# Kernel optimization log

Hardware: AMD Instinct MI355X
Metric: run time of the kernel (lower is better)

Reference implementation:

```python
import jax, jax.numpy as jnp
import numpy as np

N, D, E, TOP_K = 2048, 512, 16, 2
HID = 4 * D
EPS = 1e-10


def setup_inputs() -> dict:
    key = jax.random.key(0)
    ks = jax.random.split(key, 8)
    s = 0.02
    return {
        "x": jax.random.normal(ks[0], (N, D), dtype=jnp.float32),
        "w_norm": jnp.ones((D,), dtype=jnp.float32),
        "Wr": jax.random.normal(ks[1], (D, E), dtype=jnp.float32) * s,
        "br": jnp.zeros((E,), dtype=jnp.float32),
        "W1": jax.random.normal(ks[2], (E, D, HID), dtype=jnp.float32) * s,
        "b1": jnp.zeros((E, HID), dtype=jnp.float32),
        "W2": jax.random.normal(ks[3], (E, HID, D), dtype=jnp.float32) * s,
        "b2": jnp.zeros((E, D), dtype=jnp.float32),
    }


def reference(x, w_norm, Wr, br, W1, b1, W2, b2):
    res = x
    # RMSNorm over feature dim (dim=1 in the torch code for 2D input)
    rms = jnp.sqrt(jnp.mean(x * x, axis=1, keepdims=True) + EPS)
    xn = w_norm * (x / rms)
    # Router: top-k over expert logits, softmax over the k selected logits
    logits = xn @ Wr + br                      # [N, E]
    top_p, top_i = jax.lax.top_k(logits, TOP_K)  # [N, k]
    top_p = jax.nn.softmax(top_p, axis=-1)
    # Dense per-token expert weights [N, E] (top-k indices are distinct)
    weight = jnp.zeros((x.shape[0], E), dtype=x.dtype)
    weight = weight.at[jnp.arange(x.shape[0])[:, None], top_i].add(top_p)
    # All-expert FFN (dense reference for the routed dispatch)
    h = jnp.einsum("nd,edh->enh", xn, W1) + b1[:, None, :]   # [E, N, 4D]
    y = jnp.einsum("enh,ehd->end", jax.nn.silu(h), W2) + b2[:, None, :]  # [E, N, D]
    out = jnp.einsum("end,ne->nd", y, weight)
    return out + res
```

## Files before the change

kernel.cpp:

```cpp
#include <hip/hip_runtime.h>

#define N_TOK 2048
#define DIM   512
#define NEXP  16
#define HID   2048
#define NSLOT (N_TOK*2)

typedef __attribute__((ext_vector_type(8))) short short8;
typedef __attribute__((ext_vector_type(4))) float floatx4;

__device__ __forceinline__ ushort f2bf(float f) {
    union { float f; unsigned u; } c; c.f = f;
    unsigned u = c.u;
    unsigned r = (u + 0x7fffu + ((u >> 16) & 1u)) >> 16;
    return (ushort)r;
}
__device__ __forceinline__ float bf2f(ushort u) {
    union { unsigned u; float f; } c; c.u = ((unsigned)u) << 16;
    return c.f;
}

__device__ __forceinline__ void gl_lds16(const void* g, void* l) {
    __builtin_amdgcn_global_load_lds(
        (const __attribute__((address_space(1))) unsigned int*)g,
        (__attribute__((address_space(3))) unsigned int*)l, 16, 0, 0);
}

__device__ __forceinline__ void transpose_tile(const float* __restrict__ src,
                                               ushort* __restrict__ dst,
                                               int K, int Nn, int bx, void* smem)
{
    float* Ls = (float*)smem;
    const int NT = Nn >> 6;
    const int KT = K >> 6;
    const int nt = bx % NT; bx /= NT;
    const int kt = bx % KT; bx /= KT;
    const int e  = bx;
    const int t = threadIdx.x;

    const float* sp = src + ((size_t)e * K + kt * 64) * Nn + nt * 64;
#pragma unroll
    for (int i = 0; i < 4; i++) {
        const int k  = (t >> 4) + i * 16;
        const int c4 = (t & 15) * 4;
        const float4 v = *(const float4*)(sp + (size_t)k * Nn + c4);
        Ls[k * 65 + c4 + 0] = v.x;
        Ls[k * 65 + c4 + 1] = v.y;
        Ls[k * 65 + c4 + 2] = v.z;
        Ls[k * 65 + c4 + 3] = v.w;
    }
    __syncthreads();

    ushort* dp = dst + ((size_t)e * Nn + nt * 64) * K + kt * 64;
#pragma unroll
    for (int i = 0; i < 2; i++) {
        const int n = (t >> 3) + i * 32;
        const int c = t & 7;
        unsigned w[4];
#pragma unroll
        for (int q = 0; q < 4; q++) {
            const unsigned lo = f2bf(Ls[(c * 8 + q * 2 + 0) * 65 + n]);
            const unsigned hi = f2bf(Ls[(c * 8 + q * 2 + 1) * 65 + n]);
            w[q] = lo | (hi << 16);
        }
        uint4 o = make_uint4(w[0], w[1], w[2], w[3]);
        *(uint4*)(dp + (size_t)n * K + c * 8) = o;
    }
}

__global__ __launch_bounds__(256)
void router_fused(const float* __restrict__ x, const float* __restrict__ w_norm,
                  const float* __restrict__ Wr, const float* __restrict__ br,
                  ushort* __restrict__ xn, int2* __restrict__ rec_e,
                  float2* __restrict__ rec_w)
{
    __shared__ float xs[16][516];
    __shared__ float wrT[16][516];

    const int tid  = threadIdx.x;
    const int wave = tid >> 6, lane = tid & 63;
    const int tblk = blockIdx.x * 16;

#pragma unroll
    for (int k = 0; k < 32; k++) {
        const int idx = tid + k * 256;
        wrT[idx & 15][idx >> 4] = Wr[idx];
    }

    const float4* wnp = (const float4*)w_norm;
    const float4 wa = wnp[lane], wb = wnp[lane + 64];
#pragma unroll
    for (int i = 0; i < 4; i++) {
        const int tl = wave * 4 + i, t = tblk + tl;
        const float4* xp = (const float4*)(x + (size_t)t * DIM);
        const float4 a = xp[lane], b = xp[lane + 64];
        float ss = a.x*a.x + a.y*a.y + a.z*a.z + a.w*a.w
                 + b.x*b.x + b.y*b.y + b.z*b.z + b.w*b.w;
#pragma unroll
        for (int m = 32; m >= 1; m >>= 1) ss += __shfl_xor(ss, m, 64);
        const float rinv = 1.f / sqrtf(ss * (1.f / (float)DIM) + 1e-10f);
        float4 na, nb;
        na.x = a.x * wa.x * rinv; na.y = a.y * wa.y * rinv;
        na.z = a.z * wa.z * rinv; na.w = a.w * wa.w * rinv;
        nb.x = b.x * wb.x * rinv; nb.y = b.y * wb.y * rinv;
        nb.z = b.z * wb.z * rinv; nb.w = b.w * wb.w * rinv;
        *(float4*)&xs[tl][lane * 4]       = na;
        *(float4*)&xs[tl][256 + lane * 4] = nb;
        ushort4 ua, ub;
        ua.x = f2bf(na.x); ua.y = f2bf(na.y); ua.z = f2bf(na.z); ua.w = f2bf(na.w);
        ub.x = f2bf(nb.x); ub.y = f2bf(nb.y); ub.z = f2bf(nb.z); ub.w = f2bf(nb.w);
        ushort4* xo = (ushort4*)(xn + (size_t)t * DIM);
        xo[lane] = ua; xo[lane + 64] = ub;
    }
    __syncthreads();

    const int tl = tid >> 4, e = tid & 15;
    const int t = tblk + tl;
    float acc = 0.f;
#pragma unroll 4
    for (int d = 0; d < DIM; d += 4) {
        const float4 xv = *(const float4*)&xs[tl][d];
        const float4 wv = *(const float4*)&wrT[e][d];
        acc += xv.x * wv.x + xv.y * wv.y + xv.z * wv.z + xv.w * wv.w;
    }
    const float v = acc + br[e];

    float m0 = v; int i0 = e; float m1 = -1e30f; int i1 = 16;
#pragma unroll
    for (int msk = 1; msk < 16; msk <<= 1) {
        const float om0 = __shfl_xor(m0, msk, 64); const int oi0 = __shfl_xor(i0, msk, 64);
        const float om1 = __shfl_xor(m1, msk, 64); const int oi1 = __shfl_xor(i1, msk, 64);
        const bool bf_ = (om0 > m0) || (om0 == m0 && oi0 < i0);
        const float t0m = bf_ ? om0 : m0; const int t0i = bf_ ? oi0 : i0;
        const float l0m = bf_ ? m0 : om0; const int l0i = bf_ ? i0 : oi0;
        const bool b2_ = (om1 > m1) || (om1 == m1 && oi1 < i1);
        const float t2m = b2_ ? om1 : m1; const int t2i = b2_ ? oi1 : i1;
        const bool lw = (l0m > t2m) || (l0m == t2m && l0i < t2i);
        m0 = t0m; i0 = t0i;
        m1 = lw ? l0m : t2m; i1 = lw ? l0i : t2i;
    }
    if (e == 0) {
        const float ex = expf(m1 - m0);
        const float w0 = 1.f / (1.f + ex);
        rec_e[t] = make_int2(i0, i1);
        rec_w[t] = make_float2(w0, ex * w0);
    }
}

__global__ __launch_bounds__(1024)
void plan_kernel(const int2* __restrict__ rec_e, int* __restrict__ cnt,
                 int* __restrict__ off, int* __restrict__ tok_of_slot,
                 int* __restrict__ rec_slot)
{
    __shared__ int soff[17];
    const int e = threadIdx.x >> 6;
    const int lane = threadIdx.x & 63;

    int total = 0;
    for (int c = 0; c < N_TOK / 64; c++) {
        const int2 er = rec_e[c * 64 + lane];
        const bool hit = (er.x == e) || (er.y == e);
        total += __popcll(__ballot(hit));
    }
    if (lane == 0) soff[e + 1] = total;
    __syncthreads();
    if (threadIdx.x == 0) {
        soff[0] = 0;
        for (int q = 1; q <= 16; q++) soff[q] += soff[q - 1];
    }
    __syncthreads();
    int base = soff[e];
    if (lane == 0) { cnt[e] = soff[e + 1] - base; off[e] = base; }

    for (int c = 0; c < N_TOK / 64; c++) {
        const int t = c * 64 + lane;
        const int2 er = rec_e[t];
        const bool hit = (er.x == e) || (er.y == e);
        const unsigned long long b = __ballot(hit);
        if (hit) {
            const int slot = base + __popcll(b & ((1ull << lane) - 1ull));
            tok_of_slot[slot] = t;
            const int which = (er.y == e) ? 1 : 0;
            rec_slot[t * 2 + which] = slot;
        }
        base += __popcll(b);
    }
}

__global__ __launch_bounds__(256)
void gemm1_trw2(const ushort* __restrict__ A,
                const float* __restrict__ W1, const float* __restrict__ b1,
                const int* __restrict__ cnt, const int* __restrict__ off,
                const int* __restrict__ tok_of_slot,
                ushort* __restrict__ hout,
                const float* __restrict__ w2src, ushort* __restrict__ w2dst)
{
    __shared__ __align__(16) char smem[33280];

    if (blockIdx.y >= 64) {
        const int bx = (blockIdx.y - 64) * 32 + blockIdx.x;
        transpose_tile(w2src, w2dst, HID, DIM, bx, smem);
        return;
    }

    const int flat = blockIdx.x + (blockIdx.y << 5);
    const int x = flat & 7;
    const int g = flat >> 3;
    const int e  = x + ((g >> 7) << 3);
    const int r0_ = g & 127;
    const int nb = r0_ & 31, mt = r0_ >> 5;

    const int count = cnt[e];
    if (mt * 128 >= count) return;
    const int base = off[e];
    const int rows = min(128, count - mt * 128);
    const int n0   = nb * 64;

    ushort* As_ = (ushort*)smem;
    float*  Bf_ = (float*)(smem + 16384);
    int*    toks = (int*)(smem + 32768);

    const int tid = threadIdx.x;
    if (tid < 128) {
        const int r = tid < rows ? tid : rows - 1;
        toks[tid] = tok_of_slot[base + mt * 128 + r];
    }
    __syncthreads();

    const int lane = tid & 63;
    const int wid  = tid >> 6;
    const int wm = wid >> 1, wn = wid & 1;
    const int fr = lane & 15, fg = lane >> 4;

    const int rl  = lane >> 2;
    const int sko = ((lane & 3) ^ ((lane >> 4) & 3)) * 8;

    const ushort* aptr[2];
#pragma unroll
    for (int j = 0; j < 2; j++) {
        const int s = wid * 2 + j;
        aptr[j] = A + (size_t)toks[s * 16 + rl] * DIM + sko;
    }
    const float* bptr[2];
#pragma unroll
    for (int j = 0; j < 2; j++) {
        const int s = wid * 2 + j;
        const int cs = ((lane & 15) * 4) ^ (((s >> 1) & 1) << 4);
        bptr[j] = W1 + ((size_t)e * DIM + s * 4 + (lane >> 4)) * HID + n0 + cs;
    }

    floatx4 acc[4][2];
#pragma unroll
    for (int mi = 0; mi < 4; mi++)
#pragma unroll
        for (int ni = 0; ni < 2; ni++)
#pragma unroll
            for (int r = 0; r < 4; r++) acc[mi][ni][r] = 0.f;

#define STAGE1(pb, ktn)                                                            \
    do {                                                                           \
        const int ka = (ktn) * 32;                                                 \
        const size_t kb = (size_t)(ktn) * 32 * HID;                                \
        _Pragma("unroll")                                                          \
        for (int j = 0; j < 2; j++)                                                \
            gl_lds16(aptr[j] + ka, (void*)(&As_[(pb) * 4096 + (wid * 2 + j) * 512])); \
        _Pragma("unroll")                                                          \
        for (int j = 0; j < 2; j++)                                                \
            gl_lds16(bptr[j] + kb, (void*)(&Bf_[(pb) * 2048 + (wid * 2 + j) * 256])); \
    } while (0)

    int cur = 0;
    STAGE1(0, 0);

    const int cxor = (fr >> 2) & 3;
    const int bbase = wn * 32 + fr;
    const int fgx = fg & 1;
    for (int kt = 0; kt < 16; kt++) {
        if (kt < 15) {
            STAGE1(cur ^ 1, kt + 1);
            asm volatile("s_waitcnt vmcnt(4)" ::: "memory");
        } else {
            asm volatile("s_waitcnt vmcnt(0)" ::: "memory");
        }
        __builtin_amdgcn_s_barrier();
        __builtin_amdgcn_sched_barrier(0);

        __builtin_amdgcn_s_setprio(1);
        {
            const int co = (fg ^ cxor) * 8;
            short8 af[4], bfr[2];
#pragma unroll
            for (int mi = 0; mi < 4; mi++)
                af[mi] = *(const short8*)&As_[cur * 4096 + (wm * 64 + mi * 16 + fr) * 32 + co];
#pragma unroll
            for (int ni = 0; ni < 2; ni++) {
                const int pcol = bbase + ((ni ^ fgx) << 4);
#pragma unroll
                for (int j = 0; j < 8; j++) {
                    const float f = Bf_[cur * 2048 + (fg * 8 + j) * 64 + pcol];
                    bfr[ni][j] = (short)f2bf(f);
                }
            }
#pragma unroll
            for (int mi = 0; mi < 4; mi++)
#pragma unroll
                for (int ni = 0; ni < 2; ni++)
                    acc[mi][ni] = __builtin_amdgcn_mfma_f32_16x16x32_bf16(af[mi], bfr[ni], acc[mi][ni], 0, 0, 0);
        }
        __builtin_amdgcn_s_setprio(0);

        __builtin_amdgcn_sched_barrier(0);
        __builtin_amdgcn_s_barrier();
        cur ^= 1;
    }
#undef STAGE1

#pragma unroll
    for (int ni = 0; ni < 2; ni++) {
        const int gn = n0 + wn * 32 + ni * 16 + fr;
        const float bv = b1[e * HID + gn];
#pragma unroll
        for (int mi = 0; mi < 4; mi++) {
#pragma unroll
            for (int r = 0; r < 4; r++) {
                const int lm = wm * 64 + mi * 16 + fg * 4 + r;
                if (lm < rows) {
                    const int slot = base + mt * 128 + lm;
                    float v = acc[mi][ni][r] + bv;
                    v = v / (1.f + __expf(-v));
                    hout[(size_t)slot * HID + gn] = f2bf(v);
                }
            }
        }
    }
}

__global__ __launch_bounds__(256)
void gemm2_kernel(const ushort* __restrict__ A,
                  const ushort* __restrict__ WT,
                  const int* __restrict__ cnt, const int* __restrict__ off,
                  ushort* __restrict__ yout)
{
    const int flat = blockIdx.x + (blockIdx.y << 5);
    const int x = flat & 7;
    const int g = flat >> 3;
    const int G = ((g >> 5) << 3) + x;
    const int e = G >> 2, z = G & 3;
    const int idx = g & 31;
    const int mt = idx >> 3, nb = idx & 7;

    const int count = cnt[e];
    if (mt * 128 >= count) return;
    const int base = off[e];
    const int rows = min(128, count - mt * 128);
    const int n0   = nb * 64;
    const int kbeg = z * 512;
    ushort* yp = yout + (size_t)z * NSLOT * DIM;

    __shared__ __align__(16) ushort As[2][128 * 32];
    __shared__ __align__(16) ushort Bs[2][64 * 32];
    __shared__ int toks[128];

    const int tid = threadIdx.x;
    if (tid < 128) {
        const int r = tid < rows ? tid : rows - 1;
        toks[tid] = base + mt * 128 + r;
    }
    __syncthreads();

    const int lane = tid & 63;
    const int wid  = tid >> 6;
    const int wm = wid >> 1, wn = wid & 1;
    const int fr = lane & 15, fg = lane >> 4;

    const int rl  = lane >> 2;
    const int sko = ((lane & 3) ^ ((lane >> 4) & 3)) * 8;

    const ushort* aptr[2];
#pragma unroll
    for (int j = 0; j < 2; j++) {
        const int s = wid * 2 + j;
        aptr[j] = A + (size_t)toks[s * 16 + rl] * HID + kbeg + sko;
    }
    const ushort* bptr = WT + ((size_t)e * DIM + n0 + wid * 16 + rl) * HID + kbeg + sko;

    floatx4 acc[4][2];
#pragma unroll
    for (int mi = 0; mi < 4; mi++)
#pragma unroll
        for (int ni = 0; ni < 2; ni++)
#pragma unroll
            for (int r = 0; r < 4; r++) acc[mi][ni][r] = 0.f;

#define STAGE2(pb, k0)                                                       \
    do {                                                                     \
        _Pragma("unroll")                                                    \
        for (int j = 0; j < 2; j++)                                          \
            gl_lds16(aptr[j] + (k0), (void*)(&As[pb][(wid * 2 + j) * 512])); \
        gl_lds16(bptr + (k0), (void*)(&Bs[pb][wid * 512]));                  \
    } while (0)

    int cur = 0;
    STAGE2(0, 0);

    const int cxor = (fr >> 2) & 3;
    for (int kt = 0; kt < 16; kt++) {
        if (kt < 15) {
            STAGE2(cur ^ 1, (kt + 1) * 32);
            asm volatile("s_waitcnt vmcnt(3)" ::: "memory");
        } else {
            asm volatile("s_waitcnt vmcnt(0)" ::: "memory");
        }
        __builtin_amdgcn_s_barrier();
        __builtin_amdgcn_sched_barrier(0);

        __builtin_amdgcn_s_setprio(1);
        {
            const int co = (fg ^ cxor) * 8;
            short8 af[4], bfr[2];
#pragma unroll
            for (int mi = 0; mi < 4; mi++)
                af[mi] = *(const short8*)&As[cur][(wm * 64 + mi * 16 + fr) * 32 + co];
#pragma unroll
            for (int ni = 0; ni < 2; ni++)
                bfr[ni] = *(const short8*)&Bs[cur][(wn * 32 + ni * 16 + fr) * 32 + co];
#pragma unroll
            for (int mi = 0; mi < 4; mi++)
#pragma unroll
                for (int ni = 0; ni < 2; ni++)
                    acc[mi][ni] = __builtin_amdgcn_mfma_f32_16x16x32_bf16(af[mi], bfr[ni], acc[mi][ni], 0, 0, 0);
        }
        __builtin_amdgcn_s_setprio(0);

        __builtin_amdgcn_sched_barrier(0);
        __builtin_amdgcn_s_barrier();
        cur ^= 1;
    }
#undef STAGE2

#pragma unroll
    for (int ni = 0; ni < 2; ni++) {
        const int gn = n0 + wn * 32 + ni * 16 + fr;
#pragma unroll
        for (int mi = 0; mi < 4; mi++) {
#pragma unroll
            for (int r = 0; r < 4; r++) {
                const int lm = wm * 64 + mi * 16 + fg * 4 + r;
                if (lm < rows) {
                    const int slot = base + mt * 128 + lm;
                    yp[(size_t)slot * DIM + gn] = f2bf(acc[mi][ni][r]);
                }
            }
        }
    }
}

__global__ __launch_bounds__(128)
void gather_kernel(const float* __restrict__ x, const ushort* __restrict__ ypart,
                   const float* __restrict__ b2,
                   const int2* __restrict__ rec_e, const float2* __restrict__ rec_w,
                   const int2* __restrict__ rec_slot, float* __restrict__ out)
{
    const int t = blockIdx.x;
    const int d4 = threadIdx.x * 4;
    const int2 ei = rec_e[t];
    const float2 w = rec_w[t];
    const int2 sl = rec_slot[t];
    const float4 xv  = *(const float4*)(x  + (size_t)t * DIM + d4);
    float4 s0 = make_float4(0.f, 0.f, 0.f, 0.f);
    float4 s1 = make_float4(0.f, 0.f, 0.f, 0.f);
#pragma unroll
    for (int kc = 0; kc < 4; kc++) {
        const ushort* yp = ypart + (size_t)kc * NSLOT * DIM;
        const ushort4 a = *(const ushort4*)(yp + (size_t)sl.x * DIM + d4);
        const ushort4 b = *(const ushort4*)(yp + (size_t)sl.y * DIM + d4);
        s0.x += bf2f(a.x); s0.y += bf2f(a.y); s0.z += bf2f(a.z); s0.w += bf2f(a.w);
        s1.x += bf2f(b.x); s1.y += bf2f(b.y); s1.z += bf2f(b.z); s1.w += bf2f(b.w);
    }
    const float4 b0  = *(const float4*)(b2 + (size_t)ei.x * DIM + d4);
    const float4 b1v = *(const float4*)(b2 + (size_t)ei.y * DIM + d4);
    float4 o;
    o.x = xv.x + w.x * (s0.x + b0.x) + w.y * (s1.x + b1v.x);
    o.y = xv.y + w.x * (s0.y + b0.y) + w.y * (s1.y + b1v.y);
    o.z = xv.z + w.x * (s0.z + b0.z) + w.y * (s1.z + b1v.z);
    o.w = xv.w + w.x * (s0.w + b0.w) + w.y * (s1.w + b1v.w);
    *(float4*)(out + (size_t)t * DIM + d4) = o;
}

extern "C" void kernel_launch(void* const* d_in, const int* in_sizes, int n_in,
                              void* d_out, int out_size, void* d_ws, size_t ws_size,
                              hipStream_t stream)
{
    const float* x  = (const float*)d_in[0];
    const float* wn = (const float*)d_in[1];
    const float* Wr = (const float*)d_in[2];
    const float* br = (const float*)d_in[3];
    const float* W1 = (const float*)d_in[4];
    const float* b1 = (const float*)d_in[5];
    const float* W2 = (const float*)d_in[6];
    const float* b2 = (const float*)d_in[7];
    float* out = (float*)d_out;

    char* ws = (char*)d_ws;
    ushort* W2T   = (ushort*)(ws);
    ushort* xn    = (ushort*)(ws + (32u << 20));
    ushort* h_buf = (ushort*)(ws + (34u << 20));
    ushort* y_par = (ushort*)(ws + (50u << 20));
    char* p = ws + (80u << 20);
    int*    cnt         = (int*)p;    p += 256;
    int*    off         = (int*)p;    p += 256;
    int2*   rec_e       = (int2*)p;   p += N_TOK * 8;
    float2* rec_w       = (float2*)p; p += N_TOK * 8;
    int2*   rec_slot    = (int2*)p;   p += N_TOK * 8;
    int*    tok_of_slot = (int*)p;    p += NSLOT * 4;

    router_fused<<<N_TOK / 16, 256, 0, stream>>>(x, wn, Wr, br, xn, rec_e, rec_w);

    plan_kernel<<<1, 1024, 0, stream>>>(rec_e, cnt, off, tok_of_slot, (int*)rec_slot);

    gemm1_trw2<<<dim3(32, 192), 256, 0, stream>>>(
        xn, W1, b1, cnt, off, tok_of_slot, h_buf, W2, W2T);

    gemm2_kernel<<<dim3(32, 64), 256, 0, stream>>>(h_buf, W2T, cnt, off, y_par);

    gather_kernel<<<N_TOK, 128, 0, stream>>>(x, y_par, b2, rec_e, rec_w, rec_slot, out);
}
```

Baseline: 100.7 us.

## Pre-transpose W1 to bf16 alongside plan kernel, simplify gemm1 B path

W1 is now transposed and converted to bf16 in a separate pass that also hosts the routing-plan work and the W2 transpose. gemm1 then loads bf16 K-major B tiles directly into LDS, with no per-element fp32-to-bf16 conversion and no strided LDS reads. The cost is an extra full pass over W1 (read fp32, write bf16) plus more workspace. The plan kernel shrinks to 256 threads, each wave handling 4 experts, so it can share a launch with the transpose tiles.

Result: slower. 123.8 us (+23.0%).

```diff
diff --git a/kernel.cpp b/kernel.cpp
--- a/kernel.cpp
+++ b/kernel.cpp
@@ -147,62 +147,75 @@
     }
 }
 
-__global__ __launch_bounds__(1024)
-void plan_kernel(const int2* __restrict__ rec_e, int* __restrict__ cnt,
-                 int* __restrict__ off, int* __restrict__ tok_of_slot,
-                 int* __restrict__ rec_slot)
-{
-    __shared__ int soff[17];
-    const int e = threadIdx.x >> 6;
-    const int lane = threadIdx.x & 63;
-
-    int total = 0;
-    for (int c = 0; c < N_TOK / 64; c++) {
-        const int2 er = rec_e[c * 64 + lane];
-        const bool hit = (er.x == e) || (er.y == e);
-        total += __popcll(__ballot(hit));
-    }
-    if (lane == 0) soff[e + 1] = total;
+__global__ __launch_bounds__(256)
+void plan_trw_kernel(const int2* __restrict__ rec_e, int* __restrict__ cnt,
+                     int* __restrict__ off, int* __restrict__ tok_of_slot,
+                     int* __restrict__ rec_slot,
+                     const float* __restrict__ w1src, ushort* __restrict__ w1dst,
+                     const float* __restrict__ w2src, ushort* __restrict__ w2dst)
+{
+    __shared__ __align__(16) char smem[16640];
+
+    if (blockIdx.x > 4096) {
+        transpose_tile(w2src, w2dst, HID, DIM, blockIdx.x - 4097, smem);
+        return;
+    }
+    if (blockIdx.x != 0) {
+        transpose_tile(w1src, w1dst, DIM, HID, blockIdx.x - 1, smem);
+        return;
+    }
+
+    int* soff = (int*)smem;
+    const int tid = threadIdx.x;
+    const int wv = tid >> 6, lane = tid & 63;
+
+#pragma unroll
+    for (int s = 0; s < 4; s++) {
+        const int e = wv * 4 + s;
+        int total = 0;
+        for (int c = 0; c < N_TOK / 64; c++) {
+            const int2 er = rec_e[c * 64 + lane];
+            const bool hit = (er.x == e) || (er.y == e);
+            total += __popcll(__ballot(hit));
+        }
+        if (lane == 0) soff[e + 1] = total;
+    }
     __syncthreads();
-    if (threadIdx.x == 0) {
+    if (tid == 0) {
         soff[0] = 0;
         for (int q = 1; q <= 16; q++) soff[q] += soff[q - 1];
     }
     __syncthreads();
-    int base = soff[e];
-    if (lane == 0) { cnt[e] = soff[e + 1] - base; off[e] = base; }
-
-    for (int c = 0; c < N_TOK / 64; c++) {
-        const int t = c * 64 + lane;
-        const int2 er = rec_e[t];
-        const bool hit = (er.x == e) || (er.y == e);
-        const unsigned long long b = __ballot(hit);
-        if (hit) {
-            const int slot = base + __popcll(b & ((1ull << lane) - 1ull));
-            tok_of_slot[slot] = t;
-            const int which = (er.y == e) ? 1 : 0;
-            rec_slot[t * 2 + which] = slot;
-        }
-        base += __popcll(b);
+
+#pragma unroll
+    for (int s = 0; s < 4; s++) {
+        const int e = wv * 4 + s;
+        int base = soff[e];
+        if (lane == 0) { cnt[e] = soff[e + 1] - base; off[e] = base; }
+        for (int c = 0; c < N_TOK / 64; c++) {
+            const int t = c * 64 + lane;
+            const int2 er = rec_e[t];
+            const bool hit = (er.x == e) || (er.y == e);
+            const unsigned long long b = __ballot(hit);
+            if (hit) {
+                const int slot = base + __popcll(b & ((1ull << lane) - 1ull));
+                tok_of_slot[slot] = t;
+                const int which = (er.y == e) ? 1 : 0;
+                rec_slot[t * 2 + which] = slot;
+            }
+            base += __popcll(b);
+        }
     }
 }
 
 __global__ __launch_bounds__(256)
-void gemm1_trw2(const ushort* __restrict__ A,
-                const float* __restrict__ W1, const float* __restrict__ b1,
-                const int* __restrict__ cnt, const int* __restrict__ off,
-                const int* __restrict__ tok_of_slot,
-                ushort* __restrict__ hout,
-                const float* __restrict__ w2src, ushort* __restrict__ w2dst)
-{
-    __shared__ __align__(16) char smem[33280];
-
-    if (blockIdx.y >= 64) {
-        const int bx = (blockIdx.y - 64) * 32 + blockIdx.x;
-        transpose_tile(w2src, w2dst, HID, DIM, bx, smem);
-        return;
-    }
-
+void gemm1_kernel(const ushort* __restrict__ A,
+                  const ushort* __restrict__ WT,
+                  const float* __restrict__ bias,
+                  const int* __restrict__ cnt, const int* __restrict__ off,
+                  const int* __restrict__ tok_of_slot,
+                  ushort* __restrict__ hout)
+{
     const int flat = blockIdx.x + (blockIdx.y << 5);
     const int x = flat & 7;
     const int g = flat >> 3;
@@ -216,9 +229,9 @@
     const int rows = min(128, count - mt * 128);
     const int n0   = nb * 64;
 
-    ushort* As_ = (ushort*)smem;
-    float*  Bf_ = (float*)(smem + 16384);
-    int*    toks = (int*)(smem + 32768);
+    __shared__ __align__(16) ushort As[2][128 * 32];
+    __shared__ __align__(16) ushort Bs[2][64 * 32];
+    __shared__ int toks[128];
 
     const int tid = threadIdx.x;
     if (tid < 128) {
@@ -241,13 +254,7 @@
         const int s = wid * 2 + j;
         aptr[j] = A + (size_t)toks[s * 16 + rl] * DIM + sko;
     }
-    const float* bptr[2];
-#pragma unroll
-    for (int j = 0; j < 2; j++) {
-        const int s = wid * 2 + j;
-        const int cs = ((lane & 15) * 4) ^ (((s >> 1) & 1) << 4);
-        bptr[j] = W1 + ((size_t)e * DIM + s * 4 + (lane >> 4)) * HID + n0 + cs;
-    }
+    const ushort* bptr = WT + ((size_t)e * HID + n0 + wid * 16 + rl) * DIM + sko;
 
     floatx4 acc[4][2];
 #pragma unroll
@@ -257,28 +264,22 @@
 #pragma unroll
             for (int r = 0; r < 4; r++) acc[mi][ni][r] = 0.f;
 
-#define STAGE1(pb, ktn)                                                            \
-    do {                                                                           \
-        const int ka = (ktn) * 32;                                                 \
-        const size_t kb = (size_t)(ktn) * 32 * HID;                                \
-        _Pragma("unroll")                                                          \
-        for (int j = 0; j < 2; j++)                                                \
-            gl_lds16(aptr[j] + ka, (void*)(&As_[(pb) * 4096 + (wid * 2 + j) * 512])); \
-        _Pragma("unroll")                                                          \
-        for (int j = 0; j < 2; j++)                                                \
-            gl_lds16(bptr[j] + kb, (void*)(&Bf_[(pb) * 2048 + (wid * 2 + j) * 256])); \
+#define STAGE1(pb, k0)                                                       \
+    do {                                                                     \
+        _Pragma("unroll")                                                    \
+        for (int j = 0; j < 2; j++)                                          \
+            gl_lds16(aptr[j] + (k0), (void*)(&As[pb][(wid * 2 + j) * 512])); \
+        gl_lds16(bptr + (k0), (void*)(&Bs[pb][wid * 512]));                  \
     } while (0)
 
     int cur = 0;
     STAGE1(0, 0);
 
     const int cxor = (fr >> 2) & 3;
-    const int bbase = wn * 32 + fr;
-    const int fgx = fg & 1;
     for (int kt = 0; kt < 16; kt++) {
         if (kt < 15) {
-            STAGE1(cur ^ 1, kt + 1);
-            asm volatile("s_waitcnt vmcnt(4)" ::: "memory");
+            STAGE1(cur ^ 1, (kt + 1) * 32);
+            asm volatile("s_waitcnt vmcnt(3)" ::: "memory");
         } else {
             asm volatile("s_waitcnt vmcnt(0)" ::: "memory");
         }
@@ -291,16 +292,10 @@
             short8 af[4], bfr[2];
 #pragma unroll
             for (int mi = 0; mi < 4; mi++)
-                af[mi] = *(const short8*)&As_[cur * 4096 + (wm * 64 + mi * 16 + fr) * 32 + co];
-#pragma unroll
-            for (int ni = 0; ni < 2; ni++) {
-                const int pcol = bbase + ((ni ^ fgx) << 4);
-#pragma unroll
-                for (int j = 0; j < 8; j++) {
-                    const float f = Bf_[cur * 2048 + (fg * 8 + j) * 64 + pcol];
-                    bfr[ni][j] = (short)f2bf(f);
-                }
-            }
+                af[mi] = *(const short8*)&As[cur][(wm * 64 + mi * 16 + fr) * 32 + co];
+#pragma unroll
+            for (int ni = 0; ni < 2; ni++)
+                bfr[ni] = *(const short8*)&Bs[cur][(wn * 32 + ni * 16 + fr) * 32 + co];
 #pragma unroll
             for (int mi = 0; mi < 4; mi++)
 #pragma unroll
@@ -318,7 +313,7 @@
 #pragma unroll
     for (int ni = 0; ni < 2; ni++) {
         const int gn = n0 + wn * 32 + ni * 16 + fr;
-        const float bv = b1[e * HID + gn];
+        const float bv = bias[e * HID + gn];
 #pragma unroll
         for (int mi = 0; mi < 4; mi++) {
 #pragma unroll
@@ -502,11 +497,12 @@
     float* out = (float*)d_out;
 
     char* ws = (char*)d_ws;
-    ushort* W2T   = (ushort*)(ws);
-    ushort* xn    = (ushort*)(ws + (32u << 20));
-    ushort* h_buf = (ushort*)(ws + (34u << 20));
-    ushort* y_par = (ushort*)(ws + (50u << 20));
-    char* p = ws + (80u << 20);
+    ushort* W1T   = (ushort*)(ws);
+    ushort* W2T   = (ushort*)(ws + (32u << 20));
+    ushort* xn    = (ushort*)(ws + (64u << 20));
+    ushort* h_buf = (ushort*)(ws + (66u << 20));
+    ushort* y_par = (ushort*)(ws + (82u << 20));
+    char* p = ws + (100u << 20);
     int*    cnt         = (int*)p;    p += 256;
     int*    off         = (int*)p;    p += 256;
     int2*   rec_e       = (int2*)p;   p += N_TOK * 8;
@@ -516,10 +512,11 @@
 
     router_fused<<<N_TOK / 16, 256, 0, stream>>>(x, wn, Wr, br, xn, rec_e, rec_w);
 
-    plan_kernel<<<1, 1024, 0, stream>>>(rec_e, cnt, off, tok_of_slot, (int*)rec_slot);
-
-    gemm1_trw2<<<dim3(32, 192), 256, 0, stream>>>(
-        xn, W1, b1, cnt, off, tok_of_slot, h_buf, W2, W2T);
+    plan_trw_kernel<<<1 + 4096 + 4096, 256, 0, stream>>>(
+        rec_e, cnt, off, tok_of_slot, (int*)rec_slot, W1, W1T, W2, W2T);
+
+    gemm1_kernel<<<dim3(32, 64), 256, 0, stream>>>(
+        xn, W1T, b1, cnt, off, tok_of_slot, h_buf);
 
     gemm2_kernel<<<dim3(32, 64), 256, 0, stream>>>(h_buf, W2T, cnt, off, y_par);
 
```

## Convert W1 tiles to bf16 in registers before LDS store, read packed B fragments

Applied to the files above, without the earlier changes.

The B operand (fp32 W1) was previously copied global-to-LDS as fp32, and each wave converted 16 scalar LDS reads to bf16 inside the MFMA loop. Now each thread loads 8 fp32 values into registers, converts them once, and writes a swizzled short8 bf16 layout to LDS. The MFMA loop then reads B fragments as single vector loads. This halves the B footprint in LDS and removes redundant per-wave conversion. In exchange it adds register pressure and moves the B writes to after the compute barrier, which changes the vmcnt/lgkmcnt pipelining.

New measurement: 96.41 us. 4.2% less time.

```diff
diff --git a/kernel.cpp b/kernel.cpp
--- a/kernel.cpp
+++ b/kernel.cpp
@@ -195,7 +195,7 @@
                 ushort* __restrict__ hout,
                 const float* __restrict__ w2src, ushort* __restrict__ w2dst)
 {
-    __shared__ __align__(16) char smem[33280];
+    __shared__ __align__(16) char smem[25088];
 
     if (blockIdx.y >= 64) {
         const int bx = (blockIdx.y - 64) * 32 + blockIdx.x;
@@ -217,8 +217,8 @@
     const int n0   = nb * 64;
 
     ushort* As_ = (ushort*)smem;
-    float*  Bf_ = (float*)(smem + 16384);
-    int*    toks = (int*)(smem + 32768);
+    ushort* Bs_ = (ushort*)(smem + 16384);
+    int*    toks = (int*)(smem + 24576);
 
     const int tid = threadIdx.x;
     if (tid < 128) {
@@ -241,13 +241,29 @@
         const int s = wid * 2 + j;
         aptr[j] = A + (size_t)toks[s * 16 + rl] * DIM + sko;
     }
-    const float* bptr[2];
-#pragma unroll
-    for (int j = 0; j < 2; j++) {
-        const int s = wid * 2 + j;
-        const int cs = ((lane & 15) * 4) ^ (((s >> 1) & 1) << 4);
-        bptr[j] = W1 + ((size_t)e * DIM + s * 4 + (lane >> 4)) * HID + n0 + cs;
-    }
+    const float* bsrc = W1 + ((size_t)e * DIM + wid * 8) * HID + n0 + lane;
+    const int bwoff = lane * 32 + ((wid ^ ((lane >> 2) & 3)) * 8);
+
+    float breg[8];
+#define LOADB(ktn)                                                           \
+    do {                                                                     \
+        _Pragma("unroll")                                                    \
+        for (int j = 0; j < 8; j++)                                          \
+            breg[j] = bsrc[((size_t)(ktn) * 32 + j) * HID];                  \
+    } while (0)
+#define WRITEB(pb)                                                           \
+    do {                                                                     \
+        short8 bw;                                                           \
+        _Pragma("unroll")                                                    \
+        for (int j = 0; j < 8; j++) bw[j] = (short)f2bf(breg[j]);            \
+        *(short8*)&Bs_[(pb) * 2048 + bwoff] = bw;                            \
+    } while (0)
+#define STAGEA(pb, k0)                                                       \
+    do {                                                                     \
+        _Pragma("unroll")                                                    \
+        for (int j = 0; j < 2; j++)                                          \
+            gl_lds16(aptr[j] + (k0), (void*)(&As_[(pb) * 4096 + (wid * 2 + j) * 512])); \
+    } while (0)
 
     floatx4 acc[4][2];
 #pragma unroll
@@ -257,30 +273,20 @@
 #pragma unroll
             for (int r = 0; r < 4; r++) acc[mi][ni][r] = 0.f;
 
-#define STAGE1(pb, ktn)                                                            \
-    do {                                                                           \
-        const int ka = (ktn) * 32;                                                 \
-        const size_t kb = (size_t)(ktn) * 32 * HID;                                \
-        _Pragma("unroll")                                                          \
-        for (int j = 0; j < 2; j++)                                                \
-            gl_lds16(aptr[j] + ka, (void*)(&As_[(pb) * 4096 + (wid * 2 + j) * 512])); \
-        _Pragma("unroll")                                                          \
-        for (int j = 0; j < 2; j++)                                                \
-            gl_lds16(bptr[j] + kb, (void*)(&Bf_[(pb) * 2048 + (wid * 2 + j) * 256])); \
-    } while (0)
+    STAGEA(0, 0);
+    LOADB(0);
+    asm volatile("s_waitcnt vmcnt(0)" ::: "memory");
+    WRITEB(0);
 
     int cur = 0;
-    STAGE1(0, 0);
-
     const int cxor = (fr >> 2) & 3;
-    const int bbase = wn * 32 + fr;
-    const int fgx = fg & 1;
     for (int kt = 0; kt < 16; kt++) {
         if (kt < 15) {
-            STAGE1(cur ^ 1, kt + 1);
-            asm volatile("s_waitcnt vmcnt(4)" ::: "memory");
+            LOADB(kt + 1);
+            STAGEA(cur ^ 1, (kt + 1) * 32);
+            asm volatile("s_waitcnt vmcnt(10) lgkmcnt(0)" ::: "memory");
         } else {
-            asm volatile("s_waitcnt vmcnt(0)" ::: "memory");
+            asm volatile("s_waitcnt vmcnt(0) lgkmcnt(0)" ::: "memory");
         }
         __builtin_amdgcn_s_barrier();
         __builtin_amdgcn_sched_barrier(0);
@@ -293,14 +299,8 @@
             for (int mi = 0; mi < 4; mi++)
                 af[mi] = *(const short8*)&As_[cur * 4096 + (wm * 64 + mi * 16 + fr) * 32 + co];
 #pragma unroll
-            for (int ni = 0; ni < 2; ni++) {
-                const int pcol = bbase + ((ni ^ fgx) << 4);
-#pragma unroll
-                for (int j = 0; j < 8; j++) {
-                    const float f = Bf_[cur * 2048 + (fg * 8 + j) * 64 + pcol];
-                    bfr[ni][j] = (short)f2bf(f);
-                }
-            }
+            for (int ni = 0; ni < 2; ni++)
+                bfr[ni] = *(const short8*)&Bs_[cur * 2048 + (wn * 32 + ni * 16 + fr) * 32 + co];
 #pragma unroll
             for (int mi = 0; mi < 4; mi++)
 #pragma unroll
@@ -311,9 +311,16 @@
 
         __builtin_amdgcn_sched_barrier(0);
         __builtin_amdgcn_s_barrier();
+
+        if (kt < 15) {
+            asm volatile("s_waitcnt vmcnt(2)" ::: "memory");
+            WRITEB(cur ^ 1);
+        }
         cur ^= 1;
     }
-#undef STAGE1
+#undef LOADB
+#undef WRITEB
+#undef STAGEA
 
 #pragma unroll
     for (int ni = 0; ni < 2; ni++) {
```
